# Optimization experiments

Measured on AMD Instinct MI355X. Metric: run time of the kernel, lower is better.

Reference implementation:

```python
import jax, jax.numpy as jnp
import numpy as np

B, C, L = 16, 256, 4096   # batch, emb_dim (channels), sequence length
K = 1024                  # codebook_size
BETA = 0.25               # commitment weight


def setup_inputs() -> dict:
    key = jax.random.key(0)
    k1, k2 = jax.random.split(key)
    x = jax.random.normal(k1, (B, C, L), dtype=jnp.float32)
    codebook = jax.random.normal(k2, (K, C), dtype=jnp.float32)
    return {"x": x, "codebook": codebook}


def _l2norm(v, axis, eps=1e-12):
    return v * jax.lax.rsqrt(jnp.sum(v * v, axis=axis, keepdims=True) + eps)


def reference(x, codebook):
    # Fused, fully-batched equivalent of the original per-timestep Python loop:
    # each frame x[:, :, i] is independently quantized against the codebook, so
    # one batched nearest-codeword assignment over all (B, L) frames is exact.
    # use_cosine_sim=True: l2-normalize inputs and codewords, pick max cosine sim.
    xn = _l2norm(x, axis=1)                      # (B, C, L)
    en = _l2norm(codebook, axis=1)               # (K, C)
    sim = jnp.einsum('bcl,kc->bkl', xn, en)      # (B, K, L)
    idx = jnp.argmax(sim, axis=1)                # (B, L) nearest codeword per frame
    q = jnp.transpose(en[idx], (0, 2, 1))        # (B, C, L) quantized (normalized) frames

    # VQ loss: codebook term + beta * commitment term, averaged over all frames.
    # losses[:, i] in the torch loop is the per-call mean; losses.mean() over
    # (batch, length) equals the global mean over (B, C, L) elements.
    codebook_loss = jnp.mean((jax.lax.stop_gradient(xn) - q) ** 2)
    commit_loss = jnp.mean((xn - jax.lax.stop_gradient(q)) ** 2)
    average_loss = codebook_loss + BETA * commit_loss

    # straight-through estimator
    quantized = xn + jax.lax.stop_gradient(q - xn)
    return quantized, average_loss
```

## Files before the change

### kernel.cpp

```cpp
#include <hip/hip_runtime.h>
#include <hip/hip_bf16.h>
#include <cstdint>
#include <cstddef>

#define BB 16
#define CC 256
#define LL 4096
#define KNUM 1024
#define NFRM (BB * LL)
#define QCAP 1536
#define BAND 0.012f

static const size_t NOUT = (size_t)BB * CC * LL;

typedef __attribute__((ext_vector_type(8))) short short8v;
typedef __attribute__((ext_vector_type(4))) float f32x4;
typedef __attribute__((ext_vector_type(8))) __bf16 bf16x8;

__device__ __forceinline__ f32x4 mfma16(short8v a, short8v b, f32x4 c) {
    return __builtin_amdgcn_mfma_f32_16x16x32_bf16(
        __builtin_bit_cast(bf16x8, a), __builtin_bit_cast(bf16x8, b), c, 0, 0, 0);
}

__device__ __forceinline__ short bf16bits(float v) {
    __hip_bfloat16 h = __float2bfloat16(v);
    return *reinterpret_cast<short*>(&h);
}

__device__ __forceinline__ unsigned long long packkey(float s, int k) {
    unsigned int sb = __float_as_uint(s);
    sb = (sb & 0x80000000u) ? ~sb : (sb | 0x80000000u);
    return ((unsigned long long)sb << 32) | (unsigned long long)(1023 - k);
}

__global__ void k_cbnorm(const float* __restrict__ cb, float* __restrict__ en,
                         float* __restrict__ enorm2, short* __restrict__ enh) {
    __shared__ double wsum[4];
    const int k = blockIdx.x, c = threadIdx.x;
    float v = cb[(size_t)k * CC + c];
    double d = (double)v * (double)v;
#pragma unroll
    for (int m = 32; m >= 1; m >>= 1) d += __shfl_down(d, m);
    const int wv = c >> 6, ln = c & 63;
    if (ln == 0) wsum[wv] = d;
    __syncthreads();
    const double tot = wsum[0] + wsum[1] + wsum[2] + wsum[3];
    const float s32 = (float)tot;
    const float rn = 1.0f / sqrtf(s32 + 1e-12f);
    const float e = v * rn;
    en[(size_t)k * CC + c] = e;
    enh[((size_t)((k >> 8) * 8 + (c >> 5)) << 13) + ((k & 255) << 5) + (c & 31)] =
        bf16bits(e);
    double e2 = (double)e * (double)e;
#pragma unroll
    for (int m = 32; m >= 1; m >>= 1) e2 += __shfl_down(e2, m);
    __syncthreads();
    if (ln == 0) wsum[wv] = e2;
    __syncthreads();
    if (c == 0) enorm2[k] = (float)(wsum[0] + wsum[1] + wsum[2] + wsum[3]);
}

#define BLOAD(dst, kcv, csv)                                                   \
    {                                                                          \
        const short* bt = enh + ((size_t)((kcv) * 8 + (csv)) << 13);           \
        _Pragma("unroll")                                                      \
        for (int kt = 0; kt < 4; ++kt)                                         \
            dst[kt] = *(const short8v*)&bt[(w * 64 + kt * 16 + lr) * 32 +      \
                                           lg * 8];                            \
    }

__global__ __launch_bounds__(256, 2) void k_mega(
    const float* __restrict__ x, const float* __restrict__ en,
    const float* __restrict__ enorm2, const short* __restrict__ enh,
    float* __restrict__ out, float* __restrict__ loss) {
    __shared__ char U[64 * 257 * 4];
    __shared__ double red[4][64];
    __shared__ float rns_l[64];
    __shared__ float nxn_l[64];
    __shared__ unsigned short qd[QCAP];
    __shared__ unsigned long long pk_l[64];
    __shared__ float wmax[256];
    __shared__ int qn;

    short* A = (short*)U;
    float* xn = (float*)U;

    const int tid = threadIdx.x;
    const int w = tid >> 6;
    const int l = tid & 63;
    const int lr = l & 15, lg = l >> 4;
    const int b = blockIdx.x >> 6;
    const int l0 = (blockIdx.x & 63) << 6;
    const float* xp = x + (size_t)b * CC * LL + l0 + l;

    {
        double s0 = 0.0, s1 = 0.0, s2 = 0.0, s3 = 0.0;
#pragma unroll 4
        for (int i = 0; i < 64; i += 4) {
            int c = w * 64 + i;
            float v0 = xp[(size_t)(c + 0) * LL];
            float v1 = xp[(size_t)(c + 1) * LL];
            float v2 = xp[(size_t)(c + 2) * LL];
            float v3 = xp[(size_t)(c + 3) * LL];
            s0 += (double)v0 * v0; s1 += (double)v1 * v1;
            s2 += (double)v2 * v2; s3 += (double)v3 * v3;
        }
        red[w][l] = (s0 + s1) + (s2 + s3);
    }
    __syncthreads();
    if (tid < 64) {
        double tot = (red[0][tid] + red[1][tid]) + (red[2][tid] + red[3][tid]);
        const float s32 = (float)tot;
        const float rn = 1.0f / sqrtf(s32 + 1e-12f);
        rns_l[tid] = rn;
        nxn_l[tid] = s32 * rn * rn;
        pk_l[tid] = 0ull;
    }
    if (tid == 0) qn = 0;
    __syncthreads();

    {
        const float rn = rns_l[l];
#pragma unroll
        for (int i8 = 0; i8 < 8; ++i8) {
            int cb = w * 64 + i8 * 8;
            short8v o;
#pragma unroll
            for (int j = 0; j < 8; ++j)
                o[j] = bf16bits(xp[(size_t)(cb + j) * LL] * rn);
            *(short8v*)&A[(l * 256 + cb) ^ ((l & 7) << 3)] = o;
        }
    }
    __syncthreads();

    float runmax[4][4];
#pragma unroll
    for (int i = 0; i < 4; ++i)
#pragma unroll
        for (int r = 0; r < 4; ++r) runmax[i][r] = -3e38f;

    short8v breg[2][4];
    BLOAD(breg[0], 0, 0);

    for (int kc = 0; kc < 4; ++kc) {
        f32x4 acc[4][4];
#pragma unroll
        for (int ft = 0; ft < 4; ++ft)
#pragma unroll
            for (int kt = 0; kt < 4; ++kt) acc[ft][kt] = (f32x4){0.f, 0.f, 0.f, 0.f};

#pragma unroll
        for (int cs = 0; cs < 8; ++cs) {
            const int cur = cs & 1, nxt = cur ^ 1;
            if (cs < 7) {
                BLOAD(breg[nxt], kc, cs + 1);
            } else if (kc < 3) {
                BLOAD(breg[nxt], kc + 1, 0);
            }
            short8v af[4];
#pragma unroll
            for (int ft = 0; ft < 4; ++ft) {
                int fr = ft * 16 + lr;
                af[ft] = *(const short8v*)&A[(fr * 256 + cs * 32 + lg * 8) ^ ((lr & 7) << 3)];
            }
#pragma unroll
            for (int kt = 0; kt < 4; ++kt)
#pragma unroll
                for (int ft = 0; ft < 4; ++ft)
                    acc[ft][kt] = mfma16(af[ft], breg[cur][kt], acc[ft][kt]);
        }

        float mloc[4][4];
#pragma unroll
        for (int ft = 0; ft < 4; ++ft)
#pragma unroll
            for (int r = 0; r < 4; ++r) {
                float m = fmaxf(fmaxf(acc[ft][0][r], acc[ft][1][r]),
                                fmaxf(acc[ft][2][r], acc[ft][3][r]));
#pragma unroll
                for (int mm = 1; mm < 16; mm <<= 1) m = fmaxf(m, __shfl_xor(m, mm));
                mloc[ft][r] = m;
            }
        if (lr == 0) {
#pragma unroll
            for (int ft = 0; ft < 4; ++ft)
#pragma unroll
                for (int r = 0; r < 4; ++r)
                    wmax[((w * 4 + ft) * 4 + lg) * 4 + r] = mloc[ft][r];
        }
        __syncthreads();
#pragma unroll
        for (int ft = 0; ft < 4; ++ft) {
#pragma unroll
            for (int r = 0; r < 4; ++r) {
                float gm = fmaxf(
                    fmaxf(wmax[((0 * 4 + ft) * 4 + lg) * 4 + r],
                          wmax[((1 * 4 + ft) * 4 + lg) * 4 + r]),
                    fmaxf(wmax[((2 * 4 + ft) * 4 + lg) * 4 + r],
                          wmax[((3 * 4 + ft) * 4 + lg) * 4 + r]));
                float rm = fmaxf(runmax[ft][r], gm);
                runmax[ft][r] = rm;
                const float thr = rm - BAND;
                const int fl = ft * 16 + lg * 4 + r;
#pragma unroll
                for (int kt = 0; kt < 4; ++kt) {
                    if (acc[ft][kt][r] >= thr) {
                        int kg = kc * 256 + w * 64 + kt * 16 + lr;
                        int slot = atomicAdd(&qn, 1);
                        if (slot < QCAP)
                            qd[slot] = (unsigned short)((fl << 10) | kg);
                    }
                }
            }
        }
        __syncthreads();
    }

    const int n = qn;

    {
        const float* xb = x + (size_t)b * CC * LL + l0;
        const int l4 = (tid & 15) << 2;
        const float r0 = rns_l[l4 + 0], r1 = rns_l[l4 + 1];
        const float r2 = rns_l[l4 + 2], r3 = rns_l[l4 + 3];
#pragma unroll 4
        for (int it = 0; it < 16; ++it) {
            const int c = it * 16 + (tid >> 4);
            f32x4 v = *(const f32x4*)&xb[(size_t)c * LL + l4];
            xn[(l4 + 0) * 257 + c] = v[0] * r0;
            xn[(l4 + 1) * 257 + c] = v[1] * r1;
            xn[(l4 + 2) * 257 + c] = v[2] * r2;
            xn[(l4 + 3) * 257 + c] = v[3] * r3;
        }
    }
    __syncthreads();

    if (n <= QCAP) {
        for (int e = tid; e < n; e += 256) {
            const unsigned short ent = qd[e];
            const int fl = ent >> 10, k = ent & 1023;
            const f32x4* er4 = (const f32x4*)(en + (size_t)k * CC);
            const float* xr = &xn[fl * 257];
            float s = 0.f;
#pragma unroll 8
            for (int c4 = 0; c4 < 64; ++c4) {
                f32x4 ev = er4[c4];
                s = fmaf(xr[c4 * 4 + 0], ev[0], s);
                s = fmaf(xr[c4 * 4 + 1], ev[1], s);
                s = fmaf(xr[c4 * 4 + 2], ev[2], s);
                s = fmaf(xr[c4 * 4 + 3], ev[3], s);
            }
            atomicMax(&pk_l[fl], packkey(s, k));
        }
    } else {
        const int fl = tid >> 2, q = tid & 3;
        const float* xr = &xn[fl * 257];
        unsigned long long best = 0ull;
        for (int k = q * 256; k < q * 256 + 256; ++k) {
            const f32x4* er4 = (const f32x4*)(en + (size_t)k * CC);
            float s = 0.f;
#pragma unroll 8
            for (int c4 = 0; c4 < 64; ++c4) {
                f32x4 ev = er4[c4];
                s = fmaf(xr[c4 * 4 + 0], ev[0], s);
                s = fmaf(xr[c4 * 4 + 1], ev[1], s);
                s = fmaf(xr[c4 * 4 + 2], ev[2], s);
                s = fmaf(xr[c4 * 4 + 3], ev[3], s);
            }
            unsigned long long key = packkey(s, k);
            if (key > best) best = key;
        }
        atomicMax(&pk_l[fl], best);
    }
    __syncthreads();

    float* ens = xn;
    for (int j = 0; j < 64; ++j) {
        int kwj = 1023 - (int)(pk_l[j] & 1023ull);
        ens[j * 257 + tid] = en[(size_t)kwj * CC + tid];
    }
    __syncthreads();
    {
        float* ob = out + (size_t)b * CC * LL + l0;
        const int fl = tid & 63, cq = tid >> 6;
#pragma unroll 4
        for (int i = 0; i < 64; ++i) {
            int c = cq * 64 + i;
            ob[(size_t)c * LL + fl] = ens[fl * 257 + c];
        }
    }
    if (tid < 64) {
        unsigned long long v = pk_l[tid];
        int kw = 1023 - (int)(v & 1023ull);
        unsigned int hi = (unsigned int)(v >> 32);
        unsigned int sb = (hi & 0x80000000u) ? (hi ^ 0x80000000u) : ~hi;
        float sim = __uint_as_float(sb);
        float part = nxn_l[tid] + enorm2[kw] - 2.0f * sim;
#pragma unroll
        for (int m = 32; m >= 1; m >>= 1) part += __shfl_xor(part, m);
        if (tid == 0) atomicAdd(loss, part * (1.25f / 16777216.f));
    }
}

extern "C" void kernel_launch(void* const* d_in, const int* in_sizes, int n_in,
                              void* d_out, int out_size, void* d_ws, size_t ws_size,
                              hipStream_t stream) {
    const float* x = (const float*)d_in[0];
    const float* cb = (const float*)d_in[1];
    float* out = (float*)d_out;
    char* ws = (char*)d_ws;

    float* en     = (float*)(ws);
    float* enorm2 = (float*)(ws + 0x100000);
    short* enh    = (short*)(ws + 0x101000);

    hipMemsetAsync(out + NOUT, 0, sizeof(float), stream);

    k_cbnorm<<<KNUM, 256, 0, stream>>>(cb, en, enorm2, enh);
    k_mega<<<BB * (LL / 64), 256, 0, stream>>>(x, en, enorm2, enh, out, out + NOUT);
}
```

Measured before the change: 141.0 us.

## Widen per-wave codeword tile to 128 and skip candidate scan via wave vote

Each wave now covers 128 codewords per pass instead of 64, so the codebook sweep takes 2 outer iterations instead of 4. This halves the block barriers and LDS max-reductions, and lets each LDS A-fragment load feed twice as many MFMAs. The candidate-collection loop is also guarded by a wave-wide __any check on the wave's own max, so waves with no codeword near the running max skip the per-element compare and atomic work. In exchange, accumulator and B-register usage doubles (128 accumulator floats plus 64 prefetch registers per thread), which risks register spills or lower occupancy under the 2-block launch bound.

```diff
diff --git a/kernel.cpp b/kernel.cpp
--- a/kernel.cpp
+++ b/kernel.cpp
@@ -60,13 +60,13 @@
     if (c == 0) enorm2[k] = (float)(wsum[0] + wsum[1] + wsum[2] + wsum[3]);
 }
 
-#define BLOAD(dst, kcv, csv)                                                   \
+#define BLOAD8(dst, kcv, csv)                                                  \
     {                                                                          \
-        const short* bt = enh + ((size_t)((kcv) * 8 + (csv)) << 13);           \
+        const short* bt = enh +                                                \
+            ((size_t)((((kcv) * 2 + (w >> 1)) * 8 + (csv)) ) << 13);           \
         _Pragma("unroll")                                                      \
-        for (int kt = 0; kt < 4; ++kt)                                         \
-            dst[kt] = *(const short8v*)&bt[(w * 64 + kt * 16 + lr) * 32 +      \
-                                           lg * 8];                            \
+        for (int kt = 0; kt < 8; ++kt)                                         \
+            dst[kt] = *(const short8v*)&bt[(kb + kt * 16 + lr) * 32 + lg * 8]; \
     }
 
 __global__ __launch_bounds__(256, 2) void k_mega(
@@ -89,6 +89,7 @@
     const int w = tid >> 6;
     const int l = tid & 63;
     const int lr = l & 15, lg = l >> 4;
+    const int kb = (w & 1) * 128;
     const int b = blockIdx.x >> 6;
     const int l0 = (blockIdx.x & 63) << 6;
     const float* xp = x + (size_t)b * CC * LL + l0 + l;
@@ -139,23 +140,24 @@
 #pragma unroll
         for (int r = 0; r < 4; ++r) runmax[i][r] = -3e38f;
 
-    short8v breg[2][4];
-    BLOAD(breg[0], 0, 0);
-
-    for (int kc = 0; kc < 4; ++kc) {
-        f32x4 acc[4][4];
+    short8v breg[2][8];
+    BLOAD8(breg[0], 0, 0);
+
+#pragma unroll
+    for (int kc = 0; kc < 2; ++kc) {
+        f32x4 acc[4][8];
 #pragma unroll
         for (int ft = 0; ft < 4; ++ft)
 #pragma unroll
-            for (int kt = 0; kt < 4; ++kt) acc[ft][kt] = (f32x4){0.f, 0.f, 0.f, 0.f};
+            for (int kt = 0; kt < 8; ++kt) acc[ft][kt] = (f32x4){0.f, 0.f, 0.f, 0.f};
 
 #pragma unroll
         for (int cs = 0; cs < 8; ++cs) {
             const int cur = cs & 1, nxt = cur ^ 1;
             if (cs < 7) {
-                BLOAD(breg[nxt], kc, cs + 1);
-            } else if (kc < 3) {
-                BLOAD(breg[nxt], kc + 1, 0);
+                BLOAD8(breg[nxt], kc, cs + 1);
+            } else if (kc < 1) {
+                BLOAD8(breg[nxt], kc + 1, 0);
             }
             short8v af[4];
 #pragma unroll
@@ -164,51 +166,47 @@
                 af[ft] = *(const short8v*)&A[(fr * 256 + cs * 32 + lg * 8) ^ ((lr & 7) << 3)];
             }
 #pragma unroll
-            for (int kt = 0; kt < 4; ++kt)
+            for (int kt = 0; kt < 8; ++kt)
 #pragma unroll
                 for (int ft = 0; ft < 4; ++ft)
                     acc[ft][kt] = mfma16(af[ft], breg[cur][kt], acc[ft][kt]);
         }
 
-        float mloc[4][4];
 #pragma unroll
         for (int ft = 0; ft < 4; ++ft)
 #pragma unroll
             for (int r = 0; r < 4; ++r) {
-                float m = fmaxf(fmaxf(acc[ft][0][r], acc[ft][1][r]),
-                                fmaxf(acc[ft][2][r], acc[ft][3][r]));
+                float m = acc[ft][0][r];
+#pragma unroll
+                for (int kt = 1; kt < 8; ++kt) m = fmaxf(m, acc[ft][kt][r]);
 #pragma unroll
                 for (int mm = 1; mm < 16; mm <<= 1) m = fmaxf(m, __shfl_xor(m, mm));
-                mloc[ft][r] = m;
-            }
-        if (lr == 0) {
-#pragma unroll
-            for (int ft = 0; ft < 4; ++ft)
-#pragma unroll
-                for (int r = 0; r < 4; ++r)
-                    wmax[((w * 4 + ft) * 4 + lg) * 4 + r] = mloc[ft][r];
-        }
+                if (lr == 0) wmax[((w * 4 + ft) * 4 + lg) * 4 + r] = m;
+            }
         __syncthreads();
 #pragma unroll
         for (int ft = 0; ft < 4; ++ft) {
 #pragma unroll
             for (int r = 0; r < 4; ++r) {
-                float gm = fmaxf(
-                    fmaxf(wmax[((0 * 4 + ft) * 4 + lg) * 4 + r],
-                          wmax[((1 * 4 + ft) * 4 + lg) * 4 + r]),
-                    fmaxf(wmax[((2 * 4 + ft) * 4 + lg) * 4 + r],
-                          wmax[((3 * 4 + ft) * 4 + lg) * 4 + r]));
+                const float w0 = wmax[((0 * 4 + ft) * 4 + lg) * 4 + r];
+                const float w1 = wmax[((1 * 4 + ft) * 4 + lg) * 4 + r];
+                const float w2 = wmax[((2 * 4 + ft) * 4 + lg) * 4 + r];
+                const float w3 = wmax[((3 * 4 + ft) * 4 + lg) * 4 + r];
+                const float gm = fmaxf(fmaxf(w0, w1), fmaxf(w2, w3));
                 float rm = fmaxf(runmax[ft][r], gm);
                 runmax[ft][r] = rm;
                 const float thr = rm - BAND;
-                const int fl = ft * 16 + lg * 4 + r;
-#pragma unroll
-                for (int kt = 0; kt < 4; ++kt) {
-                    if (acc[ft][kt][r] >= thr) {
-                        int kg = kc * 256 + w * 64 + kt * 16 + lr;
-                        int slot = atomicAdd(&qn, 1);
-                        if (slot < QCAP)
-                            qd[slot] = (unsigned short)((fl << 10) | kg);
+                const float own = wmax[((w * 4 + ft) * 4 + lg) * 4 + r];
+                if (__any(own >= thr)) {
+                    const int fl = ft * 16 + lg * 4 + r;
+#pragma unroll
+                    for (int kt = 0; kt < 8; ++kt) {
+                        if (acc[ft][kt][r] >= thr) {
+                            int kg = kc * 512 + w * 128 + kt * 16 + lr;
+                            int slot = atomicAdd(&qn, 1);
+                            if (slot < QCAP)
+                                qd[slot] = (unsigned short)((fl << 10) | kg);
+                        }
                     }
                 }
             }
```

Measured after the change: 137.6 us (median of 2 runs). -2.5%, faster.
